# Kernel tuning notes

Measured on AMD Instinct MI355X. Metric: run time of the kernel, lower is better.

The kernel has to match this reference:

```python
import jax, jax.numpy as jnp
import numpy as np

GAMMA = 12.0
NUM_NODES = 100000


def setup_inputs() -> dict:
    key = jax.random.key(0)
    k1, k2, k3, k4 = jax.random.split(key, 4)
    N, E, D = NUM_NODES, 600000, 128
    node_emb = jax.random.normal(k1, (N, D), dtype=jnp.float32)
    edge_emb = jax.random.normal(k2, (E, D), dtype=jnp.float32)
    src = jax.random.randint(k3, (E,), 0, N, dtype=jnp.int32)
    dst = jax.random.randint(k4, (E,), 0, N, dtype=jnp.int32)
    return {"node_emb": node_emb, "edge_emb": edge_emb, "src": src, "dst": dst}


def reference(node_emb, edge_emb, src, dst):
    # edge_func: score = sigmoid(gamma - ||head + rel - tail||_2), trans = head + rel
    head = node_emb[src]            # [E, D] gather
    tail = node_emb[dst]            # [E, D] gather
    trans = head + edge_emb         # [E, D]
    diff = trans - tail
    dist = jnp.sqrt(jnp.sum(diff * diff, axis=-1))          # [E] L2 norm (dist_ord=2)
    score = jax.nn.sigmoid(GAMMA - dist)                    # [E]
    # reduce_func: h[v] = sum over incoming edges of score * trans
    h = jax.ops.segment_sum(score[:, None] * trans, dst, num_segments=NUM_NODES)
    return h
```

## Files before the change

kernel.cpp:

```cpp
#include <hip/hip_runtime.h>

#define DIM 128
#define GAMMA 12.0f
#define SCAN_BLOCK 256
#define SCAN_ELEMS 1024

__global__ __launch_bounds__(256) void hist_kernel(const int* __restrict__ dst,
                                                   int* __restrict__ cnt, int E) {
    int e = blockIdx.x * (int)blockDim.x + (int)threadIdx.x;
    if (e < E) atomicAdd(&cnt[dst[e]], 1);
}

__global__ __launch_bounds__(SCAN_BLOCK) void scan_reduce_kernel(
    const int* __restrict__ cnt, int* __restrict__ blockSums, int N) {
    int b = blockIdx.x, t = threadIdx.x;
    int base = b * SCAN_ELEMS + t * 4;
    int s = 0;
    #pragma unroll
    for (int j = 0; j < 4; ++j) {
        int i = base + j;
        if (i < N) s += cnt[i];
    }
    #pragma unroll
    for (int off = 32; off > 0; off >>= 1) s += __shfl_down(s, off, 64);
    __shared__ int wsum[SCAN_BLOCK / 64];
    if ((t & 63) == 0) wsum[t >> 6] = s;
    __syncthreads();
    if (t == 0) {
        int tot = 0;
        #pragma unroll
        for (int w = 0; w < SCAN_BLOCK / 64; ++w) tot += wsum[w];
        blockSums[b] = tot;
    }
}

__global__ __launch_bounds__(SCAN_BLOCK) void scan_spine_kernel(
    int* __restrict__ blockSums, int B) {
    __shared__ int sh[SCAN_BLOCK];
    int t = threadIdx.x;
    int v = (t < B) ? blockSums[t] : 0;
    sh[t] = v;
    __syncthreads();
    for (int off = 1; off < SCAN_BLOCK; off <<= 1) {
        int u = (t >= off) ? sh[t - off] : 0;
        __syncthreads();
        sh[t] += u;
        __syncthreads();
    }
    if (t < B) blockSums[t] = sh[t] - v;
}

__global__ __launch_bounds__(SCAN_BLOCK) void scan_final_kernel(
    const int* __restrict__ blockSums, int* __restrict__ cnt_cursor,
    int* __restrict__ offs, int N) {
    __shared__ int sh[SCAN_BLOCK];
    int b = blockIdx.x, t = threadIdx.x;
    int base = b * SCAN_ELEMS + t * 4;
    int v[4];
    int s = 0;
    #pragma unroll
    for (int j = 0; j < 4; ++j) {
        int i = base + j;
        v[j] = (i < N) ? cnt_cursor[i] : 0;
        s += v[j];
    }
    sh[t] = s;
    __syncthreads();
    for (int off = 1; off < SCAN_BLOCK; off <<= 1) {
        int u = (t >= off) ? sh[t - off] : 0;
        __syncthreads();
        sh[t] += u;
        __syncthreads();
    }
    int run = blockSums[b] + sh[t] - s;
    #pragma unroll
    for (int j = 0; j < 4; ++j) {
        int i = base + j;
        if (i < N) {
            offs[i] = run;
            cnt_cursor[i] = run;
        }
        run += v[j];
    }
}

__global__ __launch_bounds__(256) void scatter_kernel(const int* __restrict__ dst,
                                                      int* __restrict__ cursor,
                                                      int* __restrict__ sorted, int E) {
    int e = blockIdx.x * (int)blockDim.x + (int)threadIdx.x;
    if (e < E) {
        int pos = atomicAdd(&cursor[dst[e]], 1);
        sorted[pos] = e;
    }
}

__global__ __launch_bounds__(256) void node_kernel(
    const float* __restrict__ node_emb,
    const float* __restrict__ edge_emb,
    const int* __restrict__ src,
    const int* __restrict__ sorted,
    const int* __restrict__ offs,
    const int* __restrict__ ends,
    float* __restrict__ out,
    int N)
{
    int wave = (blockIdx.x * (int)blockDim.x + (int)threadIdx.x) >> 6;
    int lane = threadIdx.x & 63;
    if (wave >= N) return;

    int half = lane >> 5;
    int hl   = lane & 31;

    int start = offs[wave];
    int end   = ends[wave];

    const float4* tp = (const float4*)(node_emb + (size_t)wave * DIM);
    float4 tl = tp[hl];

    float ax = 0.f, ay = 0.f, az = 0.f, aw = 0.f;

    for (int k = start + half; k < end; k += 2) {
        int e = sorted[k];
        int s = src[e];
        float4 h = ((const float4*)(node_emb + (size_t)s * DIM))[hl];
        float4 r = ((const float4*)(edge_emb + (size_t)e * DIM))[hl];
        float tx = h.x + r.x, ty = h.y + r.y, tz = h.z + r.z, tw = h.w + r.w;
        float dx = tx - tl.x, dy = ty - tl.y, dz = tz - tl.z, dw = tw - tl.w;
        float sq = dx * dx + dy * dy + dz * dz + dw * dw;
        #pragma unroll
        for (int off = 16; off > 0; off >>= 1)
            sq += __shfl_xor(sq, off, 64);
        float score = 1.0f / (1.0f + expf(sqrtf(sq) - GAMMA));
        ax += score * tx; ay += score * ty; az += score * tz; aw += score * tw;
    }

    ax += __shfl_xor(ax, 32, 64);
    ay += __shfl_xor(ay, 32, 64);
    az += __shfl_xor(az, 32, 64);
    aw += __shfl_xor(aw, 32, 64);

    if (half == 0) {
        float4* op = (float4*)(out + (size_t)wave * DIM);
        op[hl] = make_float4(ax, ay, az, aw);
    }
}

extern "C" void kernel_launch(void* const* d_in, const int* in_sizes, int n_in,
                              void* d_out, int out_size, void* d_ws, size_t ws_size,
                              hipStream_t stream) {
    const float* node_emb = (const float*)d_in[0];
    const float* edge_emb = (const float*)d_in[1];
    const int*   src      = (const int*)d_in[2];
    const int*   dst      = (const int*)d_in[3];
    float*       out      = (float*)d_out;

    int E = in_sizes[2];
    int N = out_size / DIM;
    int B = (N + SCAN_ELEMS - 1) / SCAN_ELEMS;

    int* offs      = (int*)d_ws;
    int* cursor    = offs + N;
    int* sorted    = cursor + N;
    int* blockSums = sorted + E;

    hipMemsetAsync(cursor, 0, (size_t)N * sizeof(int), stream);
    hist_kernel<<<(E + 255) / 256, 256, 0, stream>>>(dst, cursor, E);
    scan_reduce_kernel<<<B, SCAN_BLOCK, 0, stream>>>(cursor, blockSums, N);
    scan_spine_kernel<<<1, SCAN_BLOCK, 0, stream>>>(blockSums, B);
    scan_final_kernel<<<B, SCAN_BLOCK, 0, stream>>>(blockSums, cursor, offs, N);
    scatter_kernel<<<(E + 255) / 256, 256, 0, stream>>>(dst, cursor, sorted, E);

    dim3 grid(((size_t)N * 64 + 255) / 256);
    node_kernel<<<grid, 256, 0, stream>>>(node_emb, edge_emb, src, sorted,
                                          offs, cursor, out, N);
}
```

Measured before the change: 545.9 us.

## Record atomic ranks in histogram, pack edge/src pairs, process four edges per wave

The histogram pass now saves each edge's atomic rank, so the scatter pass needs no second round of atomics and writes packed (edge, src) pairs. This removes the dependent src[e] lookup in the node kernel. The node kernel now splits each wave into four 16-lane groups, each handling one edge with two float4 per lane, and prefetches the next index pair. End offsets come from offs[wave+1] instead of a cursor array. The cost is an extra rank array written and read, plus more registers per lane.

```diff
diff --git a/kernel.cpp b/kernel.cpp
--- a/kernel.cpp
+++ b/kernel.cpp
@@ -5,10 +5,11 @@
 #define SCAN_BLOCK 256
 #define SCAN_ELEMS 1024
 
-__global__ __launch_bounds__(256) void hist_kernel(const int* __restrict__ dst,
-                                                   int* __restrict__ cnt, int E) {
+__global__ __launch_bounds__(256) void hist_rank_kernel(const int* __restrict__ dst,
+                                                        int* __restrict__ cnt,
+                                                        int* __restrict__ rank, int E) {
     int e = blockIdx.x * (int)blockDim.x + (int)threadIdx.x;
-    if (e < E) atomicAdd(&cnt[dst[e]], 1);
+    if (e < E) rank[e] = atomicAdd(&cnt[dst[e]], 1);
 }
 
 __global__ __launch_bounds__(SCAN_BLOCK) void scan_reduce_kernel(
@@ -51,7 +52,7 @@
 }
 
 __global__ __launch_bounds__(SCAN_BLOCK) void scan_final_kernel(
-    const int* __restrict__ blockSums, int* __restrict__ cnt_cursor,
+    const int* __restrict__ blockSums, const int* __restrict__ cnt,
     int* __restrict__ offs, int N) {
     __shared__ int sh[SCAN_BLOCK];
     int b = blockIdx.x, t = threadIdx.x;
@@ -61,7 +62,7 @@
     #pragma unroll
     for (int j = 0; j < 4; ++j) {
         int i = base + j;
-        v[j] = (i < N) ? cnt_cursor[i] : 0;
+        v[j] = (i < N) ? cnt[i] : 0;
         s += v[j];
     }
     sh[t] = s;
@@ -76,72 +77,95 @@
     #pragma unroll
     for (int j = 0; j < 4; ++j) {
         int i = base + j;
-        if (i < N) {
-            offs[i] = run;
-            cnt_cursor[i] = run;
-        }
+        if (i < N) offs[i] = run;
         run += v[j];
     }
 }
 
-__global__ __launch_bounds__(256) void scatter_kernel(const int* __restrict__ dst,
-                                                      int* __restrict__ cursor,
-                                                      int* __restrict__ sorted, int E) {
+__global__ __launch_bounds__(256) void scatter_pack_kernel(
+    const int* __restrict__ dst, const int* __restrict__ src,
+    const int* __restrict__ rank, const int* __restrict__ offs,
+    int2* __restrict__ sorted2, int E) {
     int e = blockIdx.x * (int)blockDim.x + (int)threadIdx.x;
     if (e < E) {
-        int pos = atomicAdd(&cursor[dst[e]], 1);
-        sorted[pos] = e;
+        int d = dst[e];
+        sorted2[offs[d] + rank[e]] = make_int2(e, src[e]);
     }
 }
 
 __global__ __launch_bounds__(256) void node_kernel(
     const float* __restrict__ node_emb,
     const float* __restrict__ edge_emb,
-    const int* __restrict__ src,
-    const int* __restrict__ sorted,
+    const int2* __restrict__ sorted2,
     const int* __restrict__ offs,
-    const int* __restrict__ ends,
     float* __restrict__ out,
-    int N)
+    int N, int E)
 {
     int wave = (blockIdx.x * (int)blockDim.x + (int)threadIdx.x) >> 6;
-    int lane = threadIdx.x & 63;
+    int lane = (int)threadIdx.x & 63;
     if (wave >= N) return;
 
-    int half = lane >> 5;
-    int hl   = lane & 31;
+    int g  = lane >> 4;
+    int gl = lane & 15;
 
     int start = offs[wave];
-    int end   = ends[wave];
+    int end   = (wave + 1 < N) ? offs[wave + 1] : E;
 
     const float4* tp = (const float4*)(node_emb + (size_t)wave * DIM);
-    float4 tl = tp[hl];
-
-    float ax = 0.f, ay = 0.f, az = 0.f, aw = 0.f;
-
-    for (int k = start + half; k < end; k += 2) {
-        int e = sorted[k];
-        int s = src[e];
-        float4 h = ((const float4*)(node_emb + (size_t)s * DIM))[hl];
-        float4 r = ((const float4*)(edge_emb + (size_t)e * DIM))[hl];
-        float tx = h.x + r.x, ty = h.y + r.y, tz = h.z + r.z, tw = h.w + r.w;
-        float dx = tx - tl.x, dy = ty - tl.y, dz = tz - tl.z, dw = tw - tl.w;
-        float sq = dx * dx + dy * dy + dz * dz + dw * dw;
+    float4 t0 = tp[gl];
+    float4 t1 = tp[gl + 16];
+
+    float4 a0 = make_float4(0.f, 0.f, 0.f, 0.f);
+    float4 a1 = make_float4(0.f, 0.f, 0.f, 0.f);
+
+    int k = start + g;
+    int2 es = (k < end) ? sorted2[k] : make_int2(0, 0);
+    while (k < end) {
+        int kn = k + 4;
+        int2 esn = (kn < end) ? sorted2[kn] : es;
+
+        const float4* hp = (const float4*)(node_emb + (size_t)es.y * DIM);
+        const float4* rp = (const float4*)(edge_emb + (size_t)es.x * DIM);
+        float4 h0 = hp[gl],      h1 = hp[gl + 16];
+        float4 r0 = rp[gl],      r1 = rp[gl + 16];
+
+        float4 x0, x1;
+        x0.x = h0.x + r0.x; x0.y = h0.y + r0.y; x0.z = h0.z + r0.z; x0.w = h0.w + r0.w;
+        x1.x = h1.x + r1.x; x1.y = h1.y + r1.y; x1.z = h1.z + r1.z; x1.w = h1.w + r1.w;
+
+        float d0, sq;
+        d0 = x0.x - t0.x; sq  = d0 * d0;
+        d0 = x0.y - t0.y; sq += d0 * d0;
+        d0 = x0.z - t0.z; sq += d0 * d0;
+        d0 = x0.w - t0.w; sq += d0 * d0;
+        d0 = x1.x - t1.x; sq += d0 * d0;
+        d0 = x1.y - t1.y; sq += d0 * d0;
+        d0 = x1.z - t1.z; sq += d0 * d0;
+        d0 = x1.w - t1.w; sq += d0 * d0;
+
         #pragma unroll
-        for (int off = 16; off > 0; off >>= 1)
+        for (int off = 8; off > 0; off >>= 1)
             sq += __shfl_xor(sq, off, 64);
+
         float score = 1.0f / (1.0f + expf(sqrtf(sq) - GAMMA));
-        ax += score * tx; ay += score * ty; az += score * tz; aw += score * tw;
-    }
-
-    ax += __shfl_xor(ax, 32, 64);
-    ay += __shfl_xor(ay, 32, 64);
-    az += __shfl_xor(az, 32, 64);
-    aw += __shfl_xor(aw, 32, 64);
-
-    if (half == 0) {
+        a0.x += score * x0.x; a0.y += score * x0.y; a0.z += score * x0.z; a0.w += score * x0.w;
+        a1.x += score * x1.x; a1.y += score * x1.y; a1.z += score * x1.z; a1.w += score * x1.w;
+
+        es = esn; k = kn;
+    }
+
+    #pragma unroll
+    for (int off = 16; off <= 32; off <<= 1) {
+        a0.x += __shfl_xor(a0.x, off, 64); a0.y += __shfl_xor(a0.y, off, 64);
+        a0.z += __shfl_xor(a0.z, off, 64); a0.w += __shfl_xor(a0.w, off, 64);
+        a1.x += __shfl_xor(a1.x, off, 64); a1.y += __shfl_xor(a1.y, off, 64);
+        a1.z += __shfl_xor(a1.z, off, 64); a1.w += __shfl_xor(a1.w, off, 64);
+    }
+
+    if (g == 0) {
         float4* op = (float4*)(out + (size_t)wave * DIM);
-        op[hl] = make_float4(ax, ay, az, aw);
+        op[gl]      = a0;
+        op[gl + 16] = a1;
     }
 }
 
@@ -158,19 +182,21 @@
     int N = out_size / DIM;
     int B = (N + SCAN_ELEMS - 1) / SCAN_ELEMS;
 
-    int* offs      = (int*)d_ws;
-    int* cursor    = offs + N;
-    int* sorted    = cursor + N;
-    int* blockSums = sorted + E;
-
-    hipMemsetAsync(cursor, 0, (size_t)N * sizeof(int), stream);
-    hist_kernel<<<(E + 255) / 256, 256, 0, stream>>>(dst, cursor, E);
-    scan_reduce_kernel<<<B, SCAN_BLOCK, 0, stream>>>(cursor, blockSums, N);
+    int2* sorted2   = (int2*)d_ws;
+    int*  cnt       = (int*)(sorted2 + E);
+    int*  offs      = cnt + N;
+    int*  rank      = offs + N;
+    int*  blockSums = rank + E;
+
+    hipMemsetAsync(cnt, 0, (size_t)N * sizeof(int), stream);
+    hist_rank_kernel<<<(E + 255) / 256, 256, 0, stream>>>(dst, cnt, rank, E);
+    scan_reduce_kernel<<<B, SCAN_BLOCK, 0, stream>>>(cnt, blockSums, N);
     scan_spine_kernel<<<1, SCAN_BLOCK, 0, stream>>>(blockSums, B);
-    scan_final_kernel<<<B, SCAN_BLOCK, 0, stream>>>(blockSums, cursor, offs, N);
-    scatter_kernel<<<(E + 255) / 256, 256, 0, stream>>>(dst, cursor, sorted, E);
+    scan_final_kernel<<<B, SCAN_BLOCK, 0, stream>>>(blockSums, cnt, offs, N);
+    scatter_pack_kernel<<<(E + 255) / 256, 256, 0, stream>>>(dst, src, rank, offs,
+                                                             sorted2, E);
 
     dim3 grid(((size_t)N * 64 + 255) / 256);
-    node_kernel<<<grid, 256, 0, stream>>>(node_emb, edge_emb, src, sorted,
-                                          offs, cursor, out, N);
-}
+    node_kernel<<<grid, 256, 0, stream>>>(node_emb, edge_emb, sorted2, offs,
+                                          out, N, E);
+}
```

Result: faster. 528.2 us (-3.3%).

## Replace CSR sort-and-gather with per-edge kernel using float atomics to scatter

Applied to the files above, without the earlier changes.

Drops the histogram, three-stage scan and scatter kernels that built a dst-sorted edge list, and computes each edge independently with 16 lanes per edge. Each edge's weighted translation is accumulated into the output with unsafe float atomic adds after zeroing the output. This removes several launches and the sorting passes, but trades them for 128 float atomics per edge (about 77M), an extra tail-row gather per edge, and a non-deterministic summation order.

```diff
diff --git a/kernel.cpp b/kernel.cpp
--- a/kernel.cpp
+++ b/kernel.cpp
@@ -2,147 +2,59 @@
 
 #define DIM 128
 #define GAMMA 12.0f
-#define SCAN_BLOCK 256
-#define SCAN_ELEMS 1024
 
-__global__ __launch_bounds__(256) void hist_kernel(const int* __restrict__ dst,
-                                                   int* __restrict__ cnt, int E) {
-    int e = blockIdx.x * (int)blockDim.x + (int)threadIdx.x;
-    if (e < E) atomicAdd(&cnt[dst[e]], 1);
-}
-
-__global__ __launch_bounds__(SCAN_BLOCK) void scan_reduce_kernel(
-    const int* __restrict__ cnt, int* __restrict__ blockSums, int N) {
-    int b = blockIdx.x, t = threadIdx.x;
-    int base = b * SCAN_ELEMS + t * 4;
-    int s = 0;
-    #pragma unroll
-    for (int j = 0; j < 4; ++j) {
-        int i = base + j;
-        if (i < N) s += cnt[i];
-    }
-    #pragma unroll
-    for (int off = 32; off > 0; off >>= 1) s += __shfl_down(s, off, 64);
-    __shared__ int wsum[SCAN_BLOCK / 64];
-    if ((t & 63) == 0) wsum[t >> 6] = s;
-    __syncthreads();
-    if (t == 0) {
-        int tot = 0;
-        #pragma unroll
-        for (int w = 0; w < SCAN_BLOCK / 64; ++w) tot += wsum[w];
-        blockSums[b] = tot;
-    }
-}
-
-__global__ __launch_bounds__(SCAN_BLOCK) void scan_spine_kernel(
-    int* __restrict__ blockSums, int B) {
-    __shared__ int sh[SCAN_BLOCK];
-    int t = threadIdx.x;
-    int v = (t < B) ? blockSums[t] : 0;
-    sh[t] = v;
-    __syncthreads();
-    for (int off = 1; off < SCAN_BLOCK; off <<= 1) {
-        int u = (t >= off) ? sh[t - off] : 0;
-        __syncthreads();
-        sh[t] += u;
-        __syncthreads();
-    }
-    if (t < B) blockSums[t] = sh[t] - v;
-}
-
-__global__ __launch_bounds__(SCAN_BLOCK) void scan_final_kernel(
-    const int* __restrict__ blockSums, int* __restrict__ cnt_cursor,
-    int* __restrict__ offs, int N) {
-    __shared__ int sh[SCAN_BLOCK];
-    int b = blockIdx.x, t = threadIdx.x;
-    int base = b * SCAN_ELEMS + t * 4;
-    int v[4];
-    int s = 0;
-    #pragma unroll
-    for (int j = 0; j < 4; ++j) {
-        int i = base + j;
-        v[j] = (i < N) ? cnt_cursor[i] : 0;
-        s += v[j];
-    }
-    sh[t] = s;
-    __syncthreads();
-    for (int off = 1; off < SCAN_BLOCK; off <<= 1) {
-        int u = (t >= off) ? sh[t - off] : 0;
-        __syncthreads();
-        sh[t] += u;
-        __syncthreads();
-    }
-    int run = blockSums[b] + sh[t] - s;
-    #pragma unroll
-    for (int j = 0; j < 4; ++j) {
-        int i = base + j;
-        if (i < N) {
-            offs[i] = run;
-            cnt_cursor[i] = run;
-        }
-        run += v[j];
-    }
-}
-
-__global__ __launch_bounds__(256) void scatter_kernel(const int* __restrict__ dst,
-                                                      int* __restrict__ cursor,
-                                                      int* __restrict__ sorted, int E) {
-    int e = blockIdx.x * (int)blockDim.x + (int)threadIdx.x;
-    if (e < E) {
-        int pos = atomicAdd(&cursor[dst[e]], 1);
-        sorted[pos] = e;
-    }
-}
-
-__global__ __launch_bounds__(256) void node_kernel(
+__global__ __launch_bounds__(256) void edge_kernel(
     const float* __restrict__ node_emb,
     const float* __restrict__ edge_emb,
     const int* __restrict__ src,
-    const int* __restrict__ sorted,
-    const int* __restrict__ offs,
-    const int* __restrict__ ends,
+    const int* __restrict__ dst,
     float* __restrict__ out,
-    int N)
+    int E)
 {
-    int wave = (blockIdx.x * (int)blockDim.x + (int)threadIdx.x) >> 6;
-    int lane = threadIdx.x & 63;
-    if (wave >= N) return;
+    int e = blockIdx.x * 16 + ((int)threadIdx.x >> 4);
+    if (e >= E) return;
+    int gl = (int)threadIdx.x & 15;
 
-    int half = lane >> 5;
-    int hl   = lane & 31;
+    int s = src[e];
+    int d = dst[e];
 
-    int start = offs[wave];
-    int end   = ends[wave];
+    const float4* rp = (const float4*)(edge_emb + (size_t)e * DIM);
+    const float4* hp = (const float4*)(node_emb + (size_t)s * DIM);
+    const float4* tp = (const float4*)(node_emb + (size_t)d * DIM);
 
-    const float4* tp = (const float4*)(node_emb + (size_t)wave * DIM);
-    float4 tl = tp[hl];
+    float4 r0 = rp[gl], r1 = rp[gl + 16];
+    float4 h0 = hp[gl], h1 = hp[gl + 16];
+    float4 t0 = tp[gl], t1 = tp[gl + 16];
 
-    float ax = 0.f, ay = 0.f, az = 0.f, aw = 0.f;
+    float4 x0, x1;
+    x0.x = h0.x + r0.x; x0.y = h0.y + r0.y; x0.z = h0.z + r0.z; x0.w = h0.w + r0.w;
+    x1.x = h1.x + r1.x; x1.y = h1.y + r1.y; x1.z = h1.z + r1.z; x1.w = h1.w + r1.w;
 
-    for (int k = start + half; k < end; k += 2) {
-        int e = sorted[k];
-        int s = src[e];
-        float4 h = ((const float4*)(node_emb + (size_t)s * DIM))[hl];
-        float4 r = ((const float4*)(edge_emb + (size_t)e * DIM))[hl];
-        float tx = h.x + r.x, ty = h.y + r.y, tz = h.z + r.z, tw = h.w + r.w;
-        float dx = tx - tl.x, dy = ty - tl.y, dz = tz - tl.z, dw = tw - tl.w;
-        float sq = dx * dx + dy * dy + dz * dz + dw * dw;
-        #pragma unroll
-        for (int off = 16; off > 0; off >>= 1)
-            sq += __shfl_xor(sq, off, 64);
-        float score = 1.0f / (1.0f + expf(sqrtf(sq) - GAMMA));
-        ax += score * tx; ay += score * ty; az += score * tz; aw += score * tw;
-    }
+    float dd, sq;
+    dd = x0.x - t0.x; sq  = dd * dd;
+    dd = x0.y - t0.y; sq += dd * dd;
+    dd = x0.z - t0.z; sq += dd * dd;
+    dd = x0.w - t0.w; sq += dd * dd;
+    dd = x1.x - t1.x; sq += dd * dd;
+    dd = x1.y - t1.y; sq += dd * dd;
+    dd = x1.z - t1.z; sq += dd * dd;
+    dd = x1.w - t1.w; sq += dd * dd;
 
-    ax += __shfl_xor(ax, 32, 64);
-    ay += __shfl_xor(ay, 32, 64);
-    az += __shfl_xor(az, 32, 64);
-    aw += __shfl_xor(aw, 32, 64);
+    #pragma unroll
+    for (int off = 8; off > 0; off >>= 1)
+        sq += __shfl_xor(sq, off, 64);
 
-    if (half == 0) {
-        float4* op = (float4*)(out + (size_t)wave * DIM);
-        op[hl] = make_float4(ax, ay, az, aw);
-    }
+    float score = 1.0f / (1.0f + expf(sqrtf(sq) - GAMMA));
+
+    float* op = out + (size_t)d * DIM + gl * 4;
+    unsafeAtomicAdd(op + 0,  score * x0.x);
+    unsafeAtomicAdd(op + 1,  score * x0.y);
+    unsafeAtomicAdd(op + 2,  score * x0.z);
+    unsafeAtomicAdd(op + 3,  score * x0.w);
+    unsafeAtomicAdd(op + 64, score * x1.x);
+    unsafeAtomicAdd(op + 65, score * x1.y);
+    unsafeAtomicAdd(op + 66, score * x1.z);
+    unsafeAtomicAdd(op + 67, score * x1.w);
 }
 
 extern "C" void kernel_launch(void* const* d_in, const int* in_sizes, int n_in,
@@ -155,22 +67,9 @@
     float*       out      = (float*)d_out;
 
     int E = in_sizes[2];
-    int N = out_size / DIM;
-    int B = (N + SCAN_ELEMS - 1) / SCAN_ELEMS;
 
-    int* offs      = (int*)d_ws;
-    int* cursor    = offs + N;
-    int* sorted    = cursor + N;
-    int* blockSums = sorted + E;
+    hipMemsetAsync(out, 0, (size_t)out_size * sizeof(float), stream);
 
-    hipMemsetAsync(cursor, 0, (size_t)N * sizeof(int), stream);
-    hist_kernel<<<(E + 255) / 256, 256, 0, stream>>>(dst, cursor, E);
-    scan_reduce_kernel<<<B, SCAN_BLOCK, 0, stream>>>(cursor, blockSums, N);
-    scan_spine_kernel<<<1, SCAN_BLOCK, 0, stream>>>(blockSums, B);
-    scan_final_kernel<<<B, SCAN_BLOCK, 0, stream>>>(blockSums, cursor, offs, N);
-    scatter_kernel<<<(E + 255) / 256, 256, 0, stream>>>(dst, cursor, sorted, E);
-
-    dim3 grid(((size_t)N * 64 + 255) / 256);
-    node_kernel<<<grid, 256, 0, stream>>>(node_emb, edge_emb, src, sorted,
-                                          offs, cursor, out, N);
+    int blocks = (E + 15) / 16;
+    edge_kernel<<<blocks, 256, 0, stream>>>(node_emb, edge_emb, src, dst, out, E);
 }
```

New measurement: 1.358 ms. +148.8%, slower.
